# Performance work log

Measured on AMD Instinct MI355X. Metric: run time of the kernel, lower is better.

Reference implementation:

```python
import jax, jax.numpy as jnp
import numpy as np

D = 512
DB = D // 4          # 128
R = 4                # window radius
KB = 9               # boundary kernel
DH = D // 2          # attn mlp hidden
VOCABS = {"quality": 64, "root": 13, "bass": 13, "key": 25}
COMPS = ["quality", "root", "bass", "key"]
B, T = 4, 4096


def _ln(x, g, b, eps=1e-5):
    mu = jnp.mean(x, axis=-1, keepdims=True)
    var = jnp.var(x, axis=-1, keepdims=True)
    return (x - mu) * jax.lax.rsqrt(var + eps) * g + b


def setup_inputs() -> dict:
    key = jax.random.key(0)
    ks = jax.random.split(key, 24)
    s = 0.02
    inp = {
        "h": jax.random.normal(ks[0], (B, T, D), jnp.float32),
        # boundary head
        "w_bnd": jax.random.normal(ks[1], (D,), jnp.float32) * s,
        "b_bnd": jnp.zeros((1,), jnp.float32),
        # boundary smoother conv1d(1,1,KB)
        "conv_k": jax.random.normal(ks[2], (KB,), jnp.float32) * s,
        "conv_b": jnp.zeros((1,), jnp.float32),
        # FiLM boundary embeddings
        "e0": jnp.zeros((DB,), jnp.float32),
        "e1": jax.random.normal(ks[3], (DB,), jnp.float32) * s,
        # LayerNorms
        "ln_in_g": jnp.ones((D + DB,), jnp.float32),
        "ln_in_b": jnp.zeros((D + DB,), jnp.float32),
        "ln_h_g": jnp.ones((D,), jnp.float32),
        "ln_h_b": jnp.zeros((D,), jnp.float32),
        # FiLM mlp
        "film_w": jax.random.normal(ks[4], (D + DB, 2 * D), jnp.float32) * s,
        "film_b": jnp.zeros((2 * D,), jnp.float32),
        # per-component attn MLP (stacked over 4 comps)
        "attn_w1": jax.random.normal(ks[5], (4, D, DH), jnp.float32) * s,
        "attn_b1": jnp.zeros((4, DH), jnp.float32),
        "attn_w2": jax.random.normal(ks[6], (4, DH), jnp.float32) * s,
        "attn_b2": jnp.zeros((4,), jnp.float32),
        # per-component projector first layer (stacked)
        "proj_w1": jax.random.normal(ks[7], (4, D, D), jnp.float32) * s,
        "proj_b1": jnp.zeros((4, D), jnp.float32),
    }
    for i, c in enumerate(COMPS):
        inp[f"proj_w2_{c[0]}" if c != "key" else "proj_w2_k"] = jax.random.normal(ks[8 + i], (D, VOCABS[c]), jnp.float32) * s
        inp[f"proj_b2_{c[0]}" if c != "key" else "proj_b2_k"] = jnp.zeros((VOCABS[c],), jnp.float32)
    return inp


def reference(h, w_bnd, b_bnd, conv_k, conv_b, e0, e1,
              ln_in_g, ln_in_b, ln_h_g, ln_h_b, film_w, film_b,
              attn_w1, attn_b1, attn_w2, attn_b2, proj_w1, proj_b1,
              proj_w2_q, proj_b2_q, proj_w2_r, proj_b2_r,
              proj_w2_b, proj_b2_b, proj_w2_k, proj_b2_k):
    Bz, Tz, Dz = h.shape
    # boundary head + smoothing (conv1d, same padding) + sigmoid
    bl = jnp.einsum("btd,d->bt", h, w_bnd) + b_bnd[0]            # [B,T]
    sm = jax.lax.conv_general_dilated(bl[:, None, :], conv_k[None, None, :],
                                      (1,), [(KB // 2, KB // 2)]) + conv_b[0]
    b_soft = jax.nn.sigmoid(sm[:, 0, :])                          # [B,T]
    # FiLM
    eb = b_soft[..., None] * e1 + (1.0 - b_soft[..., None]) * e0  # [B,T,DB]
    film_in = _ln(jnp.concatenate([h, eb], axis=-1), ln_in_g, ln_in_b)
    gb = film_in @ film_w + film_b                                # [B,T,2D]
    gamma, beta = gb[..., :Dz], gb[..., Dz:]
    z = _ln(h, ln_h_g, ln_h_b) * (1.0 + gamma) + beta             # [B,T,D]
    # local windows via replicate pad + gather
    hp = jnp.pad(h, ((0, 0), (R, R), (0, 0)), mode="edge")        # [B,T+2R,D]
    idx = jnp.arange(Tz)[:, None] + jnp.arange(2 * R + 1)[None, :]  # [T,W]
    local = hp[:, idx, :]                                         # [B,T,W,D]
    c = jnp.concatenate([z[:, :, None, :], local], axis=2)        # [B,T,C,D]
    # attention pooling for all 4 components at once
    s1 = jax.nn.gelu(jnp.einsum("btcd,kdh->kbtch", c, attn_w1)
                     + attn_b1[:, None, None, None, :], approximate=False)
    scores = jnp.einsum("kbtch,kh->kbtc", s1, attn_w2) + attn_b2[:, None, None, None]
    attn = jax.nn.softmax(scores, axis=-1)                        # [K,B,T,C]
    pooled = jnp.einsum("kbtc,btcd->kbtd", attn, c)               # [K,B,T,D]
    p1 = jax.nn.gelu(jnp.einsum("kbtd,kde->kbte", pooled, proj_w1)
                     + proj_b1[:, None, None, :], approximate=False)
    lq = p1[0] @ proj_w2_q + proj_b2_q
    lr = p1[1] @ proj_w2_r + proj_b2_r
    lb = p1[2] @ proj_w2_b + proj_b2_b
    lk = p1[3] @ proj_w2_k + proj_b2_k
    return jnp.concatenate([lq, lr, lb, lk, bl[..., None]], axis=-1)  # [B,T,116]
```

## Files before the change

kernel.cpp:

```cpp
#include <hip/hip_runtime.h>
#include <hip/hip_bf16.h>

typedef unsigned short u16;
typedef unsigned int u32;

#define NR 16384
#define TT 4096

typedef __bf16 bf16_t;
typedef bf16_t bf16x8 __attribute__((ext_vector_type(8)));
typedef float f32x4 __attribute__((ext_vector_type(4)));

__device__ __forceinline__ float b2f(u16 u){ return __uint_as_float(((u32)u)<<16); }
__device__ __forceinline__ u16 f2b(float f){
  u32 u = __float_as_uint(f);
  u32 r = u + 0x7fffu + ((u>>16)&1u);
  return (u16)(r>>16);
}
__device__ __forceinline__ void up2(u32 u, float&a, float&b){
  a = __uint_as_float(u<<16);
  b = __uint_as_float(u & 0xffff0000u);
}
__device__ __forceinline__ void ld8(const u16* p, float* f){
  uint4 v = *(const uint4*)p;
  up2(v.x,f[0],f[1]); up2(v.y,f[2],f[3]);
  up2(v.z,f[4],f[5]); up2(v.w,f[6],f[7]);
}
__device__ __forceinline__ float wred(float v){
  #pragma unroll
  for(int o=32;o>0;o>>=1) v += __shfl_down(v,o,64);
  return v;
}
__device__ __forceinline__ float gelu_f(float x){
  float x2 = x*x;
  float u = x*(0.7978845608f + 0.0356774081f*x2);
  float e = __expf(2.0f*u);
  float t = 1.0f - 2.0f*__builtin_amdgcn_rcpf(e+1.0f);
  return 0.5f*x*(1.0f+t);
}
__device__ __forceinline__ void gl_lds(const void* g, void* l){
  __builtin_amdgcn_global_load_lds(
      (__attribute__((address_space(1))) void*)(void*)g,
      (__attribute__((address_space(3))) void*)l, 16, 0, 0);
}

__global__ void k_tw(const float* __restrict__ src, u16* __restrict__ dst,
                     int K, int N, long long sS, long long sD){
  __shared__ float t[32][33];
  const float* S = src + (size_t)blockIdx.z*sS;
  u16* D = dst + (size_t)blockIdx.z*sD;
  int k0 = blockIdx.y*32, n0 = blockIdx.x*32;
  int r = threadIdx.x>>5, c = threadIdx.x&31;
  #pragma unroll
  for(int p=0;p<4;p++) t[r+p*8][c] = S[(size_t)(k0+r+p*8)*N + n0 + c];
  __syncthreads();
  #pragma unroll
  for(int p=0;p<4;p++) D[(size_t)(n0+r+p*8)*K + k0 + c] = f2b(t[c][r+p*8]);
}

__global__ void k_w2c(const float* __restrict__ wq, const float* __restrict__ bq,
                      const float* __restrict__ wr, const float* __restrict__ br,
                      const float* __restrict__ wb_, const float* __restrict__ bb_,
                      const float* __restrict__ wk, const float* __restrict__ bk,
                      u16* __restrict__ W2c, float* __restrict__ b2c){
  int idx = blockIdx.x;
  int p = idx>>5, j = idx&31, tid = threadIdx.x;
  const float* Wm; const float* Bm; int V; int cofs = 0;
  if(p<=1){ Wm=wq; Bm=bq; V=64; cofs = p*32; }
  else if(p==2){ Wm=wr; Bm=br; V=13; }
  else if(p==3){ Wm=wb_; Bm=bb_; V=13; }
  else { Wm=wk; Bm=bk; V=25; }
  int c = j + cofs;
  bool valid = c < V;
  for(int k=tid;k<512;k+=256)
    W2c[(size_t)idx*512 + k] = f2b(valid ? Wm[(size_t)k*V + c] : 0.f);
  if(tid==0) b2c[idx] = valid ? Bm[c] : 0.f;
}

__global__ void k_esum(const float* __restrict__ e0, const float* __restrict__ e1,
                       float* __restrict__ es){
  int lane = threadIdx.x & 63;
  float x0 = e0[lane], x1 = e0[lane+64];
  float y0 = e1[lane], y1 = e1[lane+64];
  float s0 = x0+x1, s1 = y0+y1;
  float q0 = x0*x0+x1*x1, q1 = y0*y0+y1*y1, c = x0*y0+x1*y1;
  s0 = wred(s0); s1 = wred(s1); q0 = wred(q0); q1 = wred(q1); c = wred(c);
  if(lane==0){ es[0]=s0; es[1]=s1; es[2]=q0; es[3]=q1; es[4]=c; }
}

__global__ void k_bnd(const float* __restrict__ h, const float* __restrict__ wb,
                      const float* __restrict__ bb,
                      float* __restrict__ bl, float* __restrict__ hsum, float* __restrict__ hss,
                      u16* __restrict__ hbf, float* __restrict__ out){
  int wave = threadIdx.x>>6, lane = threadIdx.x&63;
  int n = blockIdx.x*4 + wave;
  const float4* hp = (const float4*)(h + (size_t)n*512 + lane*8);
  const float4* wp = (const float4*)(wb + lane*8);
  float4 h0 = hp[0], h1 = hp[1], w0 = wp[0], w1 = wp[1];
  float hv[8] = {h0.x,h0.y,h0.z,h0.w,h1.x,h1.y,h1.z,h1.w};
  float wv[8] = {w0.x,w0.y,w0.z,w0.w,w1.x,w1.y,w1.z,w1.w};
  float dot=0.f, s=0.f, ss=0.f;
  #pragma unroll
  for(int i=0;i<8;i++){ dot += hv[i]*wv[i]; s += hv[i]; ss += hv[i]*hv[i]; }
  u16* hd = hbf + (size_t)n*512 + lane*8;
  *(ushort4*)hd     = make_ushort4(f2b(hv[0]),f2b(hv[1]),f2b(hv[2]),f2b(hv[3]));
  *(ushort4*)(hd+4) = make_ushort4(f2b(hv[4]),f2b(hv[5]),f2b(hv[6]),f2b(hv[7]));
  dot = wred(dot); s = wred(s); ss = wred(ss);
  if(lane==0){
    float v = dot + bb[0];
    bl[n] = v; hsum[n]=s; hss[n]=ss;
    out[(size_t)n*116 + 115] = v;
  }
}

__global__ void k_conv(const float* __restrict__ bl, const float* __restrict__ ck,
                       const float* __restrict__ cb, float* __restrict__ bsoft){
  int n = blockIdx.x*256 + threadIdx.x;
  int b = n>>12, t = n&4095;
  float acc = cb[0];
  #pragma unroll
  for(int i=0;i<9;i++){
    int tt = t-4+i;
    if(tt>=0 && tt<TT) acc += bl[(b<<12)+tt]*ck[i];
  }
  bsoft[n] = 1.0f/(1.0f+expf(-acc));
}

__global__ void k_filmin(const u16* __restrict__ hbf, const float* __restrict__ bsoft,
                         const float* __restrict__ e0, const float* __restrict__ e1,
                         const float* __restrict__ es,
                         const float* __restrict__ hsum, const float* __restrict__ hss,
                         const float* __restrict__ g, const float* __restrict__ bb,
                         u16* __restrict__ fin){
  int n = blockIdx.x, tid = threadIdx.x;
  if(tid >= 160) return;
  float bs = bsoft[n], os = 1.0f - bs;
  float S  = hsum[n] + bs*es[1] + os*es[0];
  float SS = hss[n] + bs*bs*es[3] + 2.0f*bs*os*es[4] + os*os*es[2];
  float mu = S*(1.0f/640.0f);
  float var = SS*(1.0f/640.0f) - mu*mu;
  float rs = rsqrtf(var + 1e-5f);
  int d = tid*4;
  float v[4];
  if(d < 512){
    ushort4 hv = *(const ushort4*)(hbf + (size_t)n*512 + d);
    v[0]=b2f(hv.x); v[1]=b2f(hv.y); v[2]=b2f(hv.z); v[3]=b2f(hv.w);
  } else {
    float4 a = *(const float4*)(e1 + d - 512);
    float4 b0 = *(const float4*)(e0 + d - 512);
    v[0]=bs*a.x+os*b0.x; v[1]=bs*a.y+os*b0.y; v[2]=bs*a.z+os*b0.z; v[3]=bs*a.w+os*b0.w;
  }
  float4 g4 = *(const float4*)(g + d);
  float4 b4 = *(const float4*)(bb + d);
  u16 o[4];
  o[0]=f2b((v[0]-mu)*rs*g4.x+b4.x); o[1]=f2b((v[1]-mu)*rs*g4.y+b4.y);
  o[2]=f2b((v[2]-mu)*rs*g4.z+b4.z); o[3]=f2b((v[3]-mu)*rs*g4.w+b4.w);
  *(ushort4*)(fin + (size_t)n*640 + d) = make_ushort4(o[0],o[1],o[2],o[3]);
}

__global__ __launch_bounds__(256) void k_film(
    const u16* __restrict__ fin, const u16* __restrict__ WT, const float* __restrict__ fbias,
    const float* __restrict__ hsum, const float* __restrict__ hss,
    const float* __restrict__ lng, const float* __restrict__ lnb,
    const u16* __restrict__ hbf, u16* __restrict__ z){
  __shared__ __align__(16) u16 As[2][128*32];
  __shared__ __align__(16) u16 Bg[2][128*32];
  __shared__ __align__(16) u16 Bb2[2][128*32];
  int tid = threadIdx.x, wave = tid>>6, lane = tid&63;
  int cg0 = blockIdx.x*128, row0 = blockIdx.y*128;
  int wr = (wave>>1)*64, wc = (wave&1)*64;
  int lrow = lane>>2, lcol = (lane&3)*8, m15 = lane&15, q = lane>>4;
  f32x4 ag[4][4] = {}, ab[4][4] = {};
  for(int k0=0;k0<640;k0+=64){
    #pragma unroll
    for(int hh=0;hh<2;hh++){
      int kk = k0 + hh*32;
      const u16* ga = fin + (size_t)(row0 + wave*32 + lrow)*640 + kk + lcol;
      u16* la = &As[hh][wave*32*32];
      gl_lds(ga, la); gl_lds(ga + (size_t)16*640, la + 16*32);
      const u16* gg = WT + (size_t)(cg0 + wave*32 + lrow)*640 + kk + lcol;
      u16* lg = &Bg[hh][wave*32*32];
      gl_lds(gg, lg); gl_lds(gg + (size_t)16*640, lg + 16*32);
      const u16* gb2 = WT + (size_t)(cg0 + 512 + wave*32 + lrow)*640 + kk + lcol;
      u16* lb2 = &Bb2[hh][wave*32*32];
      gl_lds(gb2, lb2); gl_lds(gb2 + (size_t)16*640, lb2 + 16*32);
    }
    __syncthreads();
    #pragma unroll
    for(int hh=0;hh<2;hh++){
      bf16x8 af[4], bg[4], bb[4];
      #pragma unroll
      for(int i=0;i<4;i++){
        af[i] = *(const bf16x8*)&As[hh][(wr + i*16 + m15)*32 + q*8];
        bg[i] = *(const bf16x8*)&Bg[hh][(wc + i*16 + m15)*32 + q*8];
        bb[i] = *(const bf16x8*)&Bb2[hh][(wc + i*16 + m15)*32 + q*8];
      }
      #pragma unroll
      for(int i=0;i<4;i++)
        #pragma unroll
        for(int j=0;j<4;j++){
          ag[i][j] = __builtin_amdgcn_mfma_f32_16x16x32_bf16(bg[j], af[i], ag[i][j], 0,0,0);
          ab[i][j] = __builtin_amdgcn_mfma_f32_16x16x32_bf16(bb[j], af[i], ab[i][j], 0,0,0);
        }
    }
    __syncthreads();
  }
  #pragma unroll
  for(int i=0;i<4;i++){
    int m = row0 + wr + i*16 + m15;
    float mu = hsum[m]*(1.0f/512.0f);
    float var = hss[m]*(1.0f/512.0f) - mu*mu;
    float rs = rsqrtf(var + 1e-5f);
    #pragma unroll
    for(int j=0;j<4;j++){
      int d0 = cg0 + wc + j*16 + q*4;
      float4 g4 = *(const float4*)&lng[d0];
      float4 b4 = *(const float4*)&lnb[d0];
      float4 fg = *(const float4*)&fbias[d0];
      float4 fb = *(const float4*)&fbias[512+d0];
      float hv[4];
      { ushort4 hb4 = *(const ushort4*)(hbf + (size_t)m*512 + d0);
        hv[0]=b2f(hb4.x); hv[1]=b2f(hb4.y); hv[2]=b2f(hb4.z); hv[3]=b2f(hb4.w); }
      float gm[4] = {ag[i][j][0]+fg.x, ag[i][j][1]+fg.y, ag[i][j][2]+fg.z, ag[i][j][3]+fg.w};
      float bt[4] = {ab[i][j][0]+fb.x, ab[i][j][1]+fb.y, ab[i][j][2]+fb.z, ab[i][j][3]+fb.w};
      float gg4[4] = {g4.x,g4.y,g4.z,g4.w}, bb4[4] = {b4.x,b4.y,b4.z,b4.w};
      u16 o[4];
      #pragma unroll
      for(int r=0;r<4;r++){
        float ln = (hv[r]-mu)*rs*gg4[r] + bb4[r];
        o[r] = f2b(ln*(1.0f+gm[r]) + bt[r]);
      }
      *(ushort4*)(z + (size_t)m*512 + d0) = make_ushort4(o[0],o[1],o[2],o[3]);
    }
  }
}

__global__ __launch_bounds__(256) void k_msc(
    const u16* __restrict__ hb, const u16* __restrict__ zb,
    const u16* __restrict__ WT, const float* __restrict__ b1,
    const float* __restrict__ w2, float* __restrict__ sch, float* __restrict__ scz){
  __shared__ __align__(16) u16 As[2][64*32];
  __shared__ __align__(16) u16 Bs[2][256*32];
  int tid = threadIdx.x, wave = tid>>6, lane = tid&63;
  int bz = blockIdx.y, hk = bz>>1, src = bz&1;
  const u16* X = src ? zb : hb;
  float* sc = src ? scz : sch;
  int row0 = blockIdx.x*64;
  const u16* Wb = WT + (size_t)hk*256*512;
  int lrow = lane>>2, lcol = (lane&3)*8, m15 = lane&15, q = lane>>4;
  int wc = wave*64;
  f32x4 acc[4][4] = {};
  for(int k0=0;k0<512;k0+=64){
    #pragma unroll
    for(int hh=0;hh<2;hh++){
      int kk = k0 + hh*32;
      gl_lds(X + (size_t)(row0 + wave*16 + lrow)*512 + kk + lcol, &As[hh][wave*16*32]);
      #pragma unroll
      for(int r=0;r<4;r++)
        gl_lds(Wb + (size_t)(wave*64 + r*16 + lrow)*512 + kk + lcol,
               &Bs[hh][(wave*64 + r*16)*32]);
    }
    __syncthreads();
    #pragma unroll
    for(int hh=0;hh<2;hh++){
      bf16x8 af[4], bfr[4];
      #pragma unroll
      for(int i=0;i<4;i++){
        af[i]  = *(const bf16x8*)&As[hh][(i*16 + m15)*32 + q*8];
        bfr[i] = *(const bf16x8*)&Bs[hh][(wc + i*16 + m15)*32 + q*8];
      }
      #pragma unroll
      for(int i=0;i<4;i++)
        #pragma unroll
        for(int j=0;j<4;j++)
          acc[i][j] = __builtin_amdgcn_mfma_f32_16x16x32_bf16(bfr[j], af[i], acc[i][j], 0,0,0);
    }
    __syncthreads();
  }
  #pragma unroll
  for(int i=0;i<4;i++){
    float part = 0.f;
    #pragma unroll
    for(int j=0;j<4;j++){
      int n0 = wc + j*16 + q*4;
      float4 bias = *(const float4*)&b1[hk*256 + n0];
      float4 wv   = *(const float4*)&w2[hk*256 + n0];
      part += gelu_f(acc[i][j][0]+bias.x)*wv.x;
      part += gelu_f(acc[i][j][1]+bias.y)*wv.y;
      part += gelu_f(acc[i][j][2]+bias.z)*wv.z;
      part += gelu_f(acc[i][j][3]+bias.w)*wv.w;
    }
    part += __shfl_xor(part, 16, 64);
    part += __shfl_xor(part, 32, 64);
    if(q==0) atomicAdd(&sc[(size_t)hk*NR + row0 + i*16 + m15], part);
  }
}

__global__ __launch_bounds__(256) void k_proj(
    const u16* __restrict__ P, const u16* __restrict__ WT, const float* __restrict__ Bv,
    u16* __restrict__ X2){
  __shared__ __align__(16) u16 As[2][64*32];
  __shared__ __align__(16) u16 Bs[2][256*32];
  int tid = threadIdx.x, wave = tid>>6, lane = tid&63;
  int hk = blockIdx.z;
  int row0 = blockIdx.y*64, col0 = blockIdx.x*256;
  const u16* Xb = P + (size_t)hk*NR*512;
  const u16* Wb = WT + (size_t)hk*512*512 + (size_t)col0*512;
  const float* Bq = Bv + hk*512;
  int lrow = lane>>2, lcol = (lane&3)*8, m15 = lane&15, q = lane>>4;
  int wc = wave*64;
  f32x4 acc[4][4] = {};
  for(int k0=0;k0<512;k0+=64){
    #pragma unroll
    for(int hh=0;hh<2;hh++){
      int kk = k0 + hh*32;
      gl_lds(Xb + (size_t)(row0 + wave*16 + lrow)*512 + kk + lcol, &As[hh][wave*16*32]);
      #pragma unroll
      for(int r=0;r<4;r++)
        gl_lds(Wb + (size_t)(wave*64 + r*16 + lrow)*512 + kk + lcol,
               &Bs[hh][(wave*64 + r*16)*32]);
    }
    __syncthreads();
    #pragma unroll
    for(int hh=0;hh<2;hh++){
      bf16x8 af[4], bfr[4];
      #pragma unroll
      for(int i=0;i<4;i++){
        af[i]  = *(const bf16x8*)&As[hh][(i*16 + m15)*32 + q*8];
        bfr[i] = *(const bf16x8*)&Bs[hh][(wc + i*16 + m15)*32 + q*8];
      }
      #pragma unroll
      for(int i=0;i<4;i++)
        #pragma unroll
        for(int j=0;j<4;j++)
          acc[i][j] = __builtin_amdgcn_mfma_f32_16x16x32_bf16(bfr[j], af[i], acc[i][j], 0,0,0);
    }
    __syncthreads();
  }
  #pragma unroll
  for(int i=0;i<4;i++){
    size_t mrow = (size_t)(row0 + i*16 + m15)*2048 + hk*512;
    #pragma unroll
    for(int j=0;j<4;j++){
      int n0 = col0 + wc + j*16 + q*4;
      float4 bias = *(const float4*)&Bq[n0];
      float v0 = gelu_f(acc[i][j][0] + bias.x);
      float v1 = gelu_f(acc[i][j][1] + bias.y);
      float v2 = gelu_f(acc[i][j][2] + bias.z);
      float v3 = gelu_f(acc[i][j][3] + bias.w);
      *(ushort4*)(X2 + mrow + n0) = make_ushort4(f2b(v0),f2b(v1),f2b(v2),f2b(v3));
    }
  }
}

__global__ __launch_bounds__(256) void k_f2(
    const u16* __restrict__ X2, const u16* __restrict__ W2c, const float* __restrict__ b2c,
    float* __restrict__ out){
  __shared__ __align__(16) u16 As[2][128*32];
  __shared__ __align__(16) u16 Bs[2][32*32];
  int tid = threadIdx.x, wave = tid>>6, lane = tid&63;
  int row0 = blockIdx.x*128, p = blockIdx.y;
  int hk = (p<=1)?0:(p-1);
  int B0 = (p==0)?0:(p==1)?32:(p==2)?64:(p==3)?77:90;
  int V  = (p<=1)?32:(p==4)?25:13;
  int lrow = lane>>2, lcol = (lane&3)*8, m15 = lane&15, q = lane>>4;
  f32x4 acc[2][2] = {};
  for(int k0=0;k0<512;k0+=64){
    #pragma unroll
    for(int hh=0;hh<2;hh++){
      int kk = k0 + hh*32;
      const u16* ga = X2 + (size_t)(row0 + wave*32 + lrow)*2048 + hk*512 + kk + lcol;
      u16* la = &As[hh][wave*32*32];
      gl_lds(ga, la);
      gl_lds(ga + (size_t)16*2048, la + 16*32);
      if(wave<2)
        gl_lds(W2c + (size_t)(p*32 + wave*16 + lrow)*512 + kk + lcol, &Bs[hh][wave*16*32]);
    }
    __syncthreads();
    #pragma unroll
    for(int hh=0;hh<2;hh++){
      bf16x8 af[2], bfr[2];
      #pragma unroll
      for(int i=0;i<2;i++) af[i] = *(const bf16x8*)&As[hh][(wave*32 + i*16 + m15)*32 + q*8];
      #pragma unroll
      for(int j=0;j<2;j++) bfr[j] = *(const bf16x8*)&Bs[hh][(j*16+m15)*32 + q*8];
      #pragma unroll
      for(int i=0;i<2;i++)
        #pragma unroll
        for(int j=0;j<2;j++)
          acc[i][j] = __builtin_amdgcn_mfma_f32_16x16x32_bf16(bfr[j], af[i], acc[i][j], 0,0,0);
    }
    __syncthreads();
  }
  #pragma unroll
  for(int i=0;i<2;i++){
    size_t mrow = (size_t)(row0 + wave*32 + i*16 + m15)*116;
    #pragma unroll
    for(int j=0;j<2;j++){
      int nl0 = j*16 + q*4;
      #pragma unroll
      for(int r=0;r<4;r++){
        int nl = nl0 + r;
        if(nl < V) out[mrow + B0 + nl] = acc[i][j][r] + b2c[p*32+nl];
      }
    }
  }
}

__global__ __launch_bounds__(256) void k_pool(
    const u16* __restrict__ hb, const u16* __restrict__ z,
    const float* __restrict__ sch, const float* __restrict__ scz,
    u16* __restrict__ P){
  int wave = threadIdx.x>>6, lane = threadIdx.x&63;
  int n = blockIdx.x*4 + wave;
  int b = n>>12, t = n&4095;
  int k = lane&3, j = lane>>2;
  float s;
  if(j==0) s = scz[(size_t)k*NR+n];
  else if(j<10){
    int tc = t-5+j; tc = tc<0?0:(tc>TT-1?TT-1:tc);
    s = sch[(size_t)k*NR + (b<<12) + tc];
  } else s = -1e30f;
  float m = s;
  #pragma unroll
  for(int o=4;o<64;o<<=1) m = fmaxf(m, __shfl_xor(m,o,64));
  float e = (j<10)? expf(s-m) : 0.f;
  float sum = e;
  #pragma unroll
  for(int o=4;o<64;o<<=1) sum += __shfl_xor(sum,o,64);
  float ev = e/sum;
  int d0 = lane*8;
  float acc[4][8] = {};
  #pragma unroll
  for(int jj=0;jj<10;jj++){
    const u16* src;
    if(jj==0) src = z + (size_t)n*512 + d0;
    else {
      int tc = t-5+jj; tc = tc<0?0:(tc>TT-1?TT-1:tc);
      src = hb + ((size_t)(b<<12)+tc)*512 + d0;
    }
    float f[8]; ld8(src, f);
    float w0 = __shfl(ev, jj*4+0, 64);
    float w1 = __shfl(ev, jj*4+1, 64);
    float w2 = __shfl(ev, jj*4+2, 64);
    float w3 = __shfl(ev, jj*4+3, 64);
    #pragma unroll
    for(int i=0;i<8;i++){
      acc[0][i] += w0*f[i];
      acc[1][i] += w1*f[i];
      acc[2][i] += w2*f[i];
      acc[3][i] += w3*f[i];
    }
  }
  #pragma unroll
  for(int kk=0;kk<4;kk++){
    u16* dst = P + ((size_t)kk*NR + n)*512 + d0;
    *(ushort4*)dst     = make_ushort4(f2b(acc[kk][0]),f2b(acc[kk][1]),f2b(acc[kk][2]),f2b(acc[kk][3]));
    *(ushort4*)(dst+4) = make_ushort4(f2b(acc[kk][4]),f2b(acc[kk][5]),f2b(acc[kk][6]),f2b(acc[kk][7]));
  }
}

#define OFF_BL     0u
#define OFF_BSOFT  65536u
#define OFF_HSUM   131072u
#define OFF_HSS    196608u
#define OFF_SCH    262144u
#define OFF_SCZ    524288u
#define OFF_FIN    786432u
#define OFF_Z      55312384u
#define OFF_HBF    72089600u
#define OFF_WF     88866816u
#define OFF_WA     90177536u
#define OFF_WP     91226112u
#define OFF_P      93323264u
#define OFF_W2C    160432128u
#define OFF_B2C    160595968u
#define OFF_ES     160596608u

extern "C" void kernel_launch(void* const* d_in, const int* in_sizes, int n_in,
                              void* d_out, int out_size, void* d_ws, size_t ws_size,
                              hipStream_t stream){
  const float* h       = (const float*)d_in[0];
  const float* w_bnd   = (const float*)d_in[1];
  const float* b_bnd   = (const float*)d_in[2];
  const float* conv_k  = (const float*)d_in[3];
  const float* conv_b  = (const float*)d_in[4];
  const float* e0      = (const float*)d_in[5];
  const float* e1      = (const float*)d_in[6];
  const float* ln_in_g = (const float*)d_in[7];
  const float* ln_in_b = (const float*)d_in[8];
  const float* ln_h_g  = (const float*)d_in[9];
  const float* ln_h_b  = (const float*)d_in[10];
  const float* film_w  = (const float*)d_in[11];
  const float* film_b  = (const float*)d_in[12];
  const float* attn_w1 = (const float*)d_in[13];
  const float* attn_b1 = (const float*)d_in[14];
  const float* attn_w2 = (const float*)d_in[15];
  const float* proj_w1 = (const float*)d_in[17];
  const float* proj_b1 = (const float*)d_in[18];
  const float* wq = (const float*)d_in[19];
  const float* bq = (const float*)d_in[20];
  const float* wr = (const float*)d_in[21];
  const float* br = (const float*)d_in[22];
  const float* wb_ = (const float*)d_in[23];
  const float* bb_ = (const float*)d_in[24];
  const float* wk = (const float*)d_in[25];
  const float* bk = (const float*)d_in[26];
  float* out = (float*)d_out;
  char* ws = (char*)d_ws;

  float* bl    = (float*)(ws + OFF_BL);
  float* bsoft = (float*)(ws + OFF_BSOFT);
  float* hsum  = (float*)(ws + OFF_HSUM);
  float* hss   = (float*)(ws + OFF_HSS);
  float* sch   = (float*)(ws + OFF_SCH);
  float* scz   = (float*)(ws + OFF_SCZ);
  u16* fin     = (u16*)(ws + OFF_FIN);
  u16* X2      = (u16*)(ws + OFF_FIN);
  u16* z       = (u16*)(ws + OFF_Z);
  u16* hbf     = (u16*)(ws + OFF_HBF);
  u16* wfilm   = (u16*)(ws + OFF_WF);
  u16* wattn   = (u16*)(ws + OFF_WA);
  u16* wproj   = (u16*)(ws + OFF_WP);
  u16* P       = (u16*)(ws + OFF_P);
  u16* w2c     = (u16*)(ws + OFF_W2C);
  float* b2c   = (float*)(ws + OFF_B2C);
  float* es    = (float*)(ws + OFF_ES);

  hipMemsetAsync(ws + OFF_SCH, 0, 524288, stream);

  {
    dim3 g(1024/32, 640/32, 1);
    k_tw<<<g,256,0,stream>>>(film_w, wfilm, 640, 1024, 0, 0);
  }
  {
    dim3 g(256/32, 512/32, 4);
    k_tw<<<g,256,0,stream>>>(attn_w1, wattn, 512, 256, 512LL*256, 256LL*512);
  }
  {
    dim3 g(512/32, 512/32, 4);
    k_tw<<<g,256,0,stream>>>(proj_w1, wproj, 512, 512, 512LL*512, 512LL*512);
  }
  k_w2c<<<160,256,0,stream>>>(wq,bq,wr,br,wb_,bb_,wk,bk, w2c, b2c);
  k_esum<<<1,64,0,stream>>>(e0, e1, es);

  k_bnd<<<NR/4,256,0,stream>>>(h,w_bnd,b_bnd,bl,hsum,hss,hbf,out);
  k_conv<<<NR/256,256,0,stream>>>(bl,conv_k,conv_b,bsoft);
  k_filmin<<<NR,256,0,stream>>>(hbf,bsoft,e0,e1,es,hsum,hss,ln_in_g,ln_in_b,fin);

  {
    dim3 g(4, NR/128);
    k_film<<<g,256,0,stream>>>(fin, wfilm, film_b, hsum, hss, ln_h_g, ln_h_b, hbf, z);
  }

  {
    dim3 g(NR/64, 8);
    k_msc<<<g,256,0,stream>>>(hbf, z, wattn, attn_b1, attn_w2, sch, scz);
  }

  k_pool<<<NR/4,256,0,stream>>>(hbf,z,sch,scz,P);

  {
    dim3 g(2, NR/64, 4);
    k_proj<<<g,256,0,stream>>>(P, wproj, proj_b1, X2);
  }

  {
    dim3 g(NR/128, 5);
    k_f2<<<g,256,0,stream>>>(X2, w2c, b2c, out);
  }
}
```

Measured before the change: 387.5 us.

## Fuse projector second layer into k_proj and drop score atomics/memset

The projector's second GEMM is now computed inside k_proj. Each block covers all 512 hidden columns in two halves, stages the GELU output in LDS, and multiplies it by the small per-component output weights. This removes the X2 global round-trip and the separate k_f2 launch. k_msc now reduces its per-wave partial scores in LDS and writes them directly instead of using atomicAdd, so the memset of the score buffer goes away. In exchange k_proj has half as many blocks, more LDS, a serialized second-layer stage with W2c read straight from global, and redundant A-tile loads across the two halves.

```diff
diff --git a/kernel.cpp b/kernel.cpp
--- a/kernel.cpp
+++ b/kernel.cpp
@@ -241,6 +241,7 @@
     const float* __restrict__ w2, float* __restrict__ sch, float* __restrict__ scz){
   __shared__ __align__(16) u16 As[2][64*32];
   __shared__ __align__(16) u16 Bs[2][256*32];
+  __shared__ float pw[4][64];
   int tid = threadIdx.x, wave = tid>>6, lane = tid&63;
   int bz = blockIdx.y, hk = bz>>1, src = bz&1;
   const u16* X = src ? zb : hb;
@@ -292,116 +293,102 @@
     }
     part += __shfl_xor(part, 16, 64);
     part += __shfl_xor(part, 32, 64);
-    if(q==0) atomicAdd(&sc[(size_t)hk*NR + row0 + i*16 + m15], part);
+    if(q==0) pw[wave][i*16 + m15] = part;
+  }
+  __syncthreads();
+  if(tid < 64){
+    float s = pw[0][tid] + pw[1][tid] + pw[2][tid] + pw[3][tid];
+    sc[(size_t)hk*NR + row0 + tid] = s;
   }
 }
 
 __global__ __launch_bounds__(256) void k_proj(
     const u16* __restrict__ P, const u16* __restrict__ WT, const float* __restrict__ Bv,
-    u16* __restrict__ X2){
+    const u16* __restrict__ W2c, const float* __restrict__ b2c,
+    float* __restrict__ out){
   __shared__ __align__(16) u16 As[2][64*32];
-  __shared__ __align__(16) u16 Bs[2][256*32];
+  __shared__ __align__(16) u16 BsS[16896];
   int tid = threadIdx.x, wave = tid>>6, lane = tid&63;
-  int hk = blockIdx.z;
-  int row0 = blockIdx.y*64, col0 = blockIdx.x*256;
+  int hk = blockIdx.y;
+  int row0 = blockIdx.x*64;
   const u16* Xb = P + (size_t)hk*NR*512;
-  const u16* Wb = WT + (size_t)hk*512*512 + (size_t)col0*512;
   const float* Bq = Bv + hk*512;
+  int r2base = (hk==0) ? 0 : (hk+1)*32;
+  int nt = (hk==0) ? 4 : 2;
+  int B0 = (hk==0)?0:(hk==1)?64:(hk==2)?77:90;
+  int V  = (hk==0)?64:(hk==3)?25:13;
   int lrow = lane>>2, lcol = (lane&3)*8, m15 = lane&15, q = lane>>4;
   int wc = wave*64;
-  f32x4 acc[4][4] = {};
-  for(int k0=0;k0<512;k0+=64){
-    #pragma unroll
-    for(int hh=0;hh<2;hh++){
-      int kk = k0 + hh*32;
-      gl_lds(Xb + (size_t)(row0 + wave*16 + lrow)*512 + kk + lcol, &As[hh][wave*16*32]);
-      #pragma unroll
-      for(int r=0;r<4;r++)
-        gl_lds(Wb + (size_t)(wave*64 + r*16 + lrow)*512 + kk + lcol,
-               &Bs[hh][(wave*64 + r*16)*32]);
+  f32x4 acc2[4] = {};
+  for(int half=0; half<2; half++){
+    int c0 = half*256;
+    const u16* Wb = WT + (size_t)hk*512*512 + (size_t)c0*512;
+    f32x4 acc[4][4] = {};
+    for(int k0=0;k0<512;k0+=64){
+      #pragma unroll
+      for(int hh=0;hh<2;hh++){
+        int kk = k0 + hh*32;
+        gl_lds(Xb + (size_t)(row0 + wave*16 + lrow)*512 + kk + lcol, &As[hh][wave*16*32]);
+        u16* lb = &BsS[hh*256*32 + wave*64*32];
+        #pragma unroll
+        for(int r=0;r<4;r++)
+          gl_lds(Wb + (size_t)(wave*64 + r*16 + lrow)*512 + kk + lcol, lb + r*16*32);
+      }
+      __syncthreads();
+      #pragma unroll
+      for(int hh=0;hh<2;hh++){
+        bf16x8 af[4], bfr[4];
+        #pragma unroll
+        for(int i=0;i<4;i++){
+          af[i]  = *(const bf16x8*)&As[hh][(i*16 + m15)*32 + q*8];
+          bfr[i] = *(const bf16x8*)&BsS[hh*256*32 + (wc + i*16 + m15)*32 + q*8];
+        }
+        #pragma unroll
+        for(int i=0;i<4;i++)
+          #pragma unroll
+          for(int j=0;j<4;j++)
+            acc[i][j] = __builtin_amdgcn_mfma_f32_16x16x32_bf16(bfr[j], af[i], acc[i][j], 0,0,0);
+      }
+      __syncthreads();
+    }
+    #pragma unroll
+    for(int i=0;i<4;i++){
+      int srow = i*16 + m15;
+      #pragma unroll
+      for(int j=0;j<4;j++){
+        int sn = wc + j*16 + q*4;
+        float4 bias = *(const float4*)&Bq[c0 + sn];
+        float v0 = gelu_f(acc[i][j][0] + bias.x);
+        float v1 = gelu_f(acc[i][j][1] + bias.y);
+        float v2 = gelu_f(acc[i][j][2] + bias.z);
+        float v3 = gelu_f(acc[i][j][3] + bias.w);
+        *(ushort4*)&BsS[srow*264 + sn] = make_ushort4(f2b(v0),f2b(v1),f2b(v2),f2b(v3));
+      }
     }
     __syncthreads();
-    #pragma unroll
-    for(int hh=0;hh<2;hh++){
-      bf16x8 af[4], bfr[4];
-      #pragma unroll
-      for(int i=0;i<4;i++){
-        af[i]  = *(const bf16x8*)&As[hh][(i*16 + m15)*32 + q*8];
-        bfr[i] = *(const bf16x8*)&Bs[hh][(wc + i*16 + m15)*32 + q*8];
-      }
-      #pragma unroll
-      for(int i=0;i<4;i++)
+    for(int k2=0;k2<256;k2+=32){
+      bf16x8 af2 = *(const bf16x8*)&BsS[(wave*16 + m15)*264 + k2 + q*8];
+      #pragma unroll
+      for(int j=0;j<4;j++){
+        if(j<nt){
+          bf16x8 bf2 = *(const bf16x8*)&W2c[(size_t)(r2base + j*16 + m15)*512 + c0 + k2 + q*8];
+          acc2[j] = __builtin_amdgcn_mfma_f32_16x16x32_bf16(af2, bf2, acc2[j], 0,0,0);
+        }
+      }
+    }
+    __syncthreads();
+  }
+  #pragma unroll
+  for(int j=0;j<4;j++){
+    if(j<nt){
+      int n = j*16 + m15;
+      if(n < V){
+        float bias = b2c[r2base + n];
         #pragma unroll
-        for(int j=0;j<4;j++)
-          acc[i][j] = __builtin_amdgcn_mfma_f32_16x16x32_bf16(bfr[j], af[i], acc[i][j], 0,0,0);
-    }
-    __syncthreads();
-  }
-  #pragma unroll
-  for(int i=0;i<4;i++){
-    size_t mrow = (size_t)(row0 + i*16 + m15)*2048 + hk*512;
-    #pragma unroll
-    for(int j=0;j<4;j++){
-      int n0 = col0 + wc + j*16 + q*4;
-      float4 bias = *(const float4*)&Bq[n0];
-      float v0 = gelu_f(acc[i][j][0] + bias.x);
-      float v1 = gelu_f(acc[i][j][1] + bias.y);
-      float v2 = gelu_f(acc[i][j][2] + bias.z);
-      float v3 = gelu_f(acc[i][j][3] + bias.w);
-      *(ushort4*)(X2 + mrow + n0) = make_ushort4(f2b(v0),f2b(v1),f2b(v2),f2b(v3));
-    }
-  }
-}
-
-__global__ __launch_bounds__(256) void k_f2(
-    const u16* __restrict__ X2, const u16* __restrict__ W2c, const float* __restrict__ b2c,
-    float* __restrict__ out){
-  __shared__ __align__(16) u16 As[2][128*32];
-  __shared__ __align__(16) u16 Bs[2][32*32];
-  int tid = threadIdx.x, wave = tid>>6, lane = tid&63;
-  int row0 = blockIdx.x*128, p = blockIdx.y;
-  int hk = (p<=1)?0:(p-1);
-  int B0 = (p==0)?0:(p==1)?32:(p==2)?64:(p==3)?77:90;
-  int V  = (p<=1)?32:(p==4)?25:13;
-  int lrow = lane>>2, lcol = (lane&3)*8, m15 = lane&15, q = lane>>4;
-  f32x4 acc[2][2] = {};
-  for(int k0=0;k0<512;k0+=64){
-    #pragma unroll
-    for(int hh=0;hh<2;hh++){
-      int kk = k0 + hh*32;
-      const u16* ga = X2 + (size_t)(row0 + wave*32 + lrow)*2048 + hk*512 + kk + lcol;
-      u16* la = &As[hh][wave*32*32];
-      gl_lds(ga, la);
-      gl_lds(ga + (size_t)16*2048, la + 16*32);
-      if(wave<2)
-        gl_lds(W2c + (size_t)(p*32 + wave*16 + lrow)*512 + kk + lcol, &Bs[hh][wave*16*32]);
-    }
-    __syncthreads();
-    #pragma unroll
-    for(int hh=0;hh<2;hh++){
-      bf16x8 af[2], bfr[2];
-      #pragma unroll
-      for(int i=0;i<2;i++) af[i] = *(const bf16x8*)&As[hh][(wave*32 + i*16 + m15)*32 + q*8];
-      #pragma unroll
-      for(int j=0;j<2;j++) bfr[j] = *(const bf16x8*)&Bs[hh][(j*16+m15)*32 + q*8];
-      #pragma unroll
-      for(int i=0;i<2;i++)
-        #pragma unroll
-        for(int j=0;j<2;j++)
-          acc[i][j] = __builtin_amdgcn_mfma_f32_16x16x32_bf16(bfr[j], af[i], acc[i][j], 0,0,0);
-    }
-    __syncthreads();
-  }
-  #pragma unroll
-  for(int i=0;i<2;i++){
-    size_t mrow = (size_t)(row0 + wave*32 + i*16 + m15)*116;
-    #pragma unroll
-    for(int j=0;j<2;j++){
-      int nl0 = j*16 + q*4;
-      #pragma unroll
-      for(int r=0;r<4;r++){
-        int nl = nl0 + r;
-        if(nl < V) out[mrow + B0 + nl] = acc[i][j][r] + b2c[p*32+nl];
+        for(int r=0;r<4;r++){
+          int row = row0 + wave*16 + q*4 + r;
+          out[(size_t)row*116 + B0 + n] = acc2[j][r] + bias;
+        }
       }
     }
   }
@@ -516,7 +503,6 @@
   float* sch   = (float*)(ws + OFF_SCH);
   float* scz   = (float*)(ws + OFF_SCZ);
   u16* fin     = (u16*)(ws + OFF_FIN);
-  u16* X2      = (u16*)(ws + OFF_FIN);
   u16* z       = (u16*)(ws + OFF_Z);
   u16* hbf     = (u16*)(ws + OFF_HBF);
   u16* wfilm   = (u16*)(ws + OFF_WF);
@@ -527,8 +513,6 @@
   float* b2c   = (float*)(ws + OFF_B2C);
   float* es    = (float*)(ws + OFF_ES);
 
-  hipMemsetAsync(ws + OFF_SCH, 0, 524288, stream);
-
   {
     dim3 g(1024/32, 640/32, 1);
     k_tw<<<g,256,0,stream>>>(film_w, wfilm, 640, 1024, 0, 0);
@@ -561,12 +545,7 @@
   k_pool<<<NR/4,256,0,stream>>>(hbf,z,sch,scz,P);
 
   {
-    dim3 g(2, NR/64, 4);
-    k_proj<<<g,256,0,stream>>>(P, wproj, proj_b1, X2);
-  }
-
-  {
-    dim3 g(NR/128, 5);
-    k_f2<<<g,256,0,stream>>>(X2, w2c, b2c, out);
-  }
-}
+    dim3 g(NR/64, 4);
+    k_proj<<<g,256,0,stream>>>(P, wproj, proj_b1, w2c, b2c, out);
+  }
+}
```

New measurement: 442.8 us. 1.14x slower.

## Software-pipeline GEMM main loops with register prefetch and drop score atomics

Applied to the files above, without the earlier changes.

The k_msc and k_proj GEMM loops previously loaded directly global-to-LDS and synchronized before computing. They now prefetch the next K-slice into registers while running MFMAs on the current LDS buffer, then store the prefetched slice to the alternate LDS buffer. That overlaps global latency with compute, at the cost of more registers and a narrower per-iteration K step. The score reduction now combines the four waves' partials in shared memory and writes them directly instead of using atomicAdd. This removes the workspace memset and the atomic traffic.

```diff
diff --git a/kernel.cpp b/kernel.cpp
--- a/kernel.cpp
+++ b/kernel.cpp
@@ -241,6 +241,7 @@
     const float* __restrict__ w2, float* __restrict__ sch, float* __restrict__ scz){
   __shared__ __align__(16) u16 As[2][64*32];
   __shared__ __align__(16) u16 Bs[2][256*32];
+  __shared__ float pw[4][64];
   int tid = threadIdx.x, wave = tid>>6, lane = tid&63;
   int bz = blockIdx.y, hk = bz>>1, src = bz&1;
   const u16* X = src ? zb : hb;
@@ -249,31 +250,50 @@
   const u16* Wb = WT + (size_t)hk*256*512;
   int lrow = lane>>2, lcol = (lane&3)*8, m15 = lane&15, q = lane>>4;
   int wc = wave*64;
+  const u16* gA = X + (size_t)(row0 + wave*16 + lrow)*512 + lcol;
+  const u16* gB = Wb + (size_t)(wave*64 + lrow)*512 + lcol;
+  int aoff = (wave*16 + lrow)*32 + lcol;
+  int boff = (wave*64 + lrow)*32 + lcol;
+  uint4 ra  = *(const uint4*)gA;
+  uint4 rb0 = *(const uint4*)(gB);
+  uint4 rb1 = *(const uint4*)(gB + 16*512);
+  uint4 rb2 = *(const uint4*)(gB + 32*512);
+  uint4 rb3 = *(const uint4*)(gB + 48*512);
+  *(uint4*)&As[0][aoff] = ra;
+  *(uint4*)&Bs[0][boff]        = rb0;
+  *(uint4*)&Bs[0][boff+16*32]  = rb1;
+  *(uint4*)&Bs[0][boff+32*32]  = rb2;
+  *(uint4*)&Bs[0][boff+48*32]  = rb3;
+  __syncthreads();
   f32x4 acc[4][4] = {};
-  for(int k0=0;k0<512;k0+=64){
-    #pragma unroll
-    for(int hh=0;hh<2;hh++){
-      int kk = k0 + hh*32;
-      gl_lds(X + (size_t)(row0 + wave*16 + lrow)*512 + kk + lcol, &As[hh][wave*16*32]);
-      #pragma unroll
-      for(int r=0;r<4;r++)
-        gl_lds(Wb + (size_t)(wave*64 + r*16 + lrow)*512 + kk + lcol,
-               &Bs[hh][(wave*64 + r*16)*32]);
-    }
-    __syncthreads();
-    #pragma unroll
-    for(int hh=0;hh<2;hh++){
-      bf16x8 af[4], bfr[4];
-      #pragma unroll
-      for(int i=0;i<4;i++){
-        af[i]  = *(const bf16x8*)&As[hh][(i*16 + m15)*32 + q*8];
-        bfr[i] = *(const bf16x8*)&Bs[hh][(wc + i*16 + m15)*32 + q*8];
-      }
-      #pragma unroll
-      for(int i=0;i<4;i++)
-        #pragma unroll
-        for(int j=0;j<4;j++)
-          acc[i][j] = __builtin_amdgcn_mfma_f32_16x16x32_bf16(bfr[j], af[i], acc[i][j], 0,0,0);
+  for(int it=0; it<16; it++){
+    int cur = it&1;
+    if(it<15){
+      int k0 = (it+1)*32;
+      ra  = *(const uint4*)(gA + k0);
+      rb0 = *(const uint4*)(gB + k0);
+      rb1 = *(const uint4*)(gB + 16*512 + k0);
+      rb2 = *(const uint4*)(gB + 32*512 + k0);
+      rb3 = *(const uint4*)(gB + 48*512 + k0);
+    }
+    bf16x8 af[4], bfr[4];
+    #pragma unroll
+    for(int i=0;i<4;i++){
+      af[i]  = *(const bf16x8*)&As[cur][(i*16 + m15)*32 + q*8];
+      bfr[i] = *(const bf16x8*)&Bs[cur][(wc + i*16 + m15)*32 + q*8];
+    }
+    #pragma unroll
+    for(int i=0;i<4;i++)
+      #pragma unroll
+      for(int j=0;j<4;j++)
+        acc[i][j] = __builtin_amdgcn_mfma_f32_16x16x32_bf16(bfr[j], af[i], acc[i][j], 0,0,0);
+    if(it<15){
+      int nxt = cur^1;
+      *(uint4*)&As[nxt][aoff] = ra;
+      *(uint4*)&Bs[nxt][boff]        = rb0;
+      *(uint4*)&Bs[nxt][boff+16*32]  = rb1;
+      *(uint4*)&Bs[nxt][boff+32*32]  = rb2;
+      *(uint4*)&Bs[nxt][boff+48*32]  = rb3;
     }
     __syncthreads();
   }
@@ -292,7 +312,12 @@
     }
     part += __shfl_xor(part, 16, 64);
     part += __shfl_xor(part, 32, 64);
-    if(q==0) atomicAdd(&sc[(size_t)hk*NR + row0 + i*16 + m15], part);
+    if(q==0) pw[wave][i*16 + m15] = part;
+  }
+  __syncthreads();
+  if(tid < 64){
+    float s = pw[0][tid] + pw[1][tid] + pw[2][tid] + pw[3][tid];
+    sc[(size_t)hk*NR + row0 + tid] = s;
   }
 }
 
@@ -309,31 +334,50 @@
   const float* Bq = Bv + hk*512;
   int lrow = lane>>2, lcol = (lane&3)*8, m15 = lane&15, q = lane>>4;
   int wc = wave*64;
+  const u16* gA = Xb + (size_t)(row0 + wave*16 + lrow)*512 + lcol;
+  const u16* gB = Wb + (size_t)(wave*64 + lrow)*512 + lcol;
+  int aoff = (wave*16 + lrow)*32 + lcol;
+  int boff = (wave*64 + lrow)*32 + lcol;
+  uint4 ra  = *(const uint4*)gA;
+  uint4 rb0 = *(const uint4*)(gB);
+  uint4 rb1 = *(const uint4*)(gB + 16*512);
+  uint4 rb2 = *(const uint4*)(gB + 32*512);
+  uint4 rb3 = *(const uint4*)(gB + 48*512);
+  *(uint4*)&As[0][aoff] = ra;
+  *(uint4*)&Bs[0][boff]        = rb0;
+  *(uint4*)&Bs[0][boff+16*32]  = rb1;
+  *(uint4*)&Bs[0][boff+32*32]  = rb2;
+  *(uint4*)&Bs[0][boff+48*32]  = rb3;
+  __syncthreads();
   f32x4 acc[4][4] = {};
-  for(int k0=0;k0<512;k0+=64){
-    #pragma unroll
-    for(int hh=0;hh<2;hh++){
-      int kk = k0 + hh*32;
-      gl_lds(Xb + (size_t)(row0 + wave*16 + lrow)*512 + kk + lcol, &As[hh][wave*16*32]);
-      #pragma unroll
-      for(int r=0;r<4;r++)
-        gl_lds(Wb + (size_t)(wave*64 + r*16 + lrow)*512 + kk + lcol,
-               &Bs[hh][(wave*64 + r*16)*32]);
-    }
-    __syncthreads();
-    #pragma unroll
-    for(int hh=0;hh<2;hh++){
-      bf16x8 af[4], bfr[4];
-      #pragma unroll
-      for(int i=0;i<4;i++){
-        af[i]  = *(const bf16x8*)&As[hh][(i*16 + m15)*32 + q*8];
-        bfr[i] = *(const bf16x8*)&Bs[hh][(wc + i*16 + m15)*32 + q*8];
-      }
-      #pragma unroll
-      for(int i=0;i<4;i++)
-        #pragma unroll
-        for(int j=0;j<4;j++)
-          acc[i][j] = __builtin_amdgcn_mfma_f32_16x16x32_bf16(bfr[j], af[i], acc[i][j], 0,0,0);
+  for(int it=0; it<16; it++){
+    int cur = it&1;
+    if(it<15){
+      int k0 = (it+1)*32;
+      ra  = *(const uint4*)(gA + k0);
+      rb0 = *(const uint4*)(gB + k0);
+      rb1 = *(const uint4*)(gB + 16*512 + k0);
+      rb2 = *(const uint4*)(gB + 32*512 + k0);
+      rb3 = *(const uint4*)(gB + 48*512 + k0);
+    }
+    bf16x8 af[4], bfr[4];
+    #pragma unroll
+    for(int i=0;i<4;i++){
+      af[i]  = *(const bf16x8*)&As[cur][(i*16 + m15)*32 + q*8];
+      bfr[i] = *(const bf16x8*)&Bs[cur][(wc + i*16 + m15)*32 + q*8];
+    }
+    #pragma unroll
+    for(int i=0;i<4;i++)
+      #pragma unroll
+      for(int j=0;j<4;j++)
+        acc[i][j] = __builtin_amdgcn_mfma_f32_16x16x32_bf16(bfr[j], af[i], acc[i][j], 0,0,0);
+    if(it<15){
+      int nxt = cur^1;
+      *(uint4*)&As[nxt][aoff] = ra;
+      *(uint4*)&Bs[nxt][boff]        = rb0;
+      *(uint4*)&Bs[nxt][boff+16*32]  = rb1;
+      *(uint4*)&Bs[nxt][boff+32*32]  = rb2;
+      *(uint4*)&Bs[nxt][boff+48*32]  = rb3;
     }
     __syncthreads();
   }
@@ -527,8 +571,6 @@
   float* b2c   = (float*)(ws + OFF_B2C);
   float* es    = (float*)(ws + OFF_ES);
 
-  hipMemsetAsync(ws + OFF_SCH, 0, 524288, stream);
-
   {
     dim3 g(1024/32, 640/32, 1);
     k_tw<<<g,256,0,stream>>>(film_w, wfilm, 640, 1024, 0, 0);
```

Result: no change. 381.7 us (-1.5%).

## Load MFMA operands straight from global into registers, drop LDS staging and atomics

Applied to the files above, without the earlier changes.

Three GEMM kernels (attention score, projector, final logits) now load their MFMA fragments directly from global memory into registers with a two-stage software prefetch. This removes the LDS staging buffers and the block-wide barriers on every K step. The score kernel also reduces per-wave partial sums in shared memory and writes each row once, so the zeroing memset and the global atomics go away. The cost is that every wave now fetches its own copy of the shared A tile from global/L2, and the B tile is read without reuse across waves. The per-lane 16-byte row-strided loads are also less coalesced than the previous LDS fills.

```diff
diff --git a/kernel.cpp b/kernel.cpp
--- a/kernel.cpp
+++ b/kernel.cpp
@@ -239,43 +239,51 @@
     const u16* __restrict__ hb, const u16* __restrict__ zb,
     const u16* __restrict__ WT, const float* __restrict__ b1,
     const float* __restrict__ w2, float* __restrict__ sch, float* __restrict__ scz){
-  __shared__ __align__(16) u16 As[2][64*32];
-  __shared__ __align__(16) u16 Bs[2][256*32];
+  __shared__ float pw[4][64];
   int tid = threadIdx.x, wave = tid>>6, lane = tid&63;
   int bz = blockIdx.y, hk = bz>>1, src = bz&1;
   const u16* X = src ? zb : hb;
   float* sc = src ? scz : sch;
   int row0 = blockIdx.x*64;
   const u16* Wb = WT + (size_t)hk*256*512;
-  int lrow = lane>>2, lcol = (lane&3)*8, m15 = lane&15, q = lane>>4;
+  int m15 = lane&15, q = lane>>4;
   int wc = wave*64;
+  const u16* pA = X  + (size_t)(row0 + m15)*512 + q*8;
+  const u16* pB = Wb + (size_t)(wc   + m15)*512 + q*8;
+  uint4 rA0[4], rB0[4], rA1[4], rB1[4];
+  #pragma unroll
+  for(int i=0;i<4;i++){
+    rA0[i] = *(const uint4*)(pA + (size_t)i*16*512);
+    rB0[i] = *(const uint4*)(pB + (size_t)i*16*512);
+  }
   f32x4 acc[4][4] = {};
-  for(int k0=0;k0<512;k0+=64){
-    #pragma unroll
-    for(int hh=0;hh<2;hh++){
-      int kk = k0 + hh*32;
-      gl_lds(X + (size_t)(row0 + wave*16 + lrow)*512 + kk + lcol, &As[hh][wave*16*32]);
-      #pragma unroll
-      for(int r=0;r<4;r++)
-        gl_lds(Wb + (size_t)(wave*64 + r*16 + lrow)*512 + kk + lcol,
-               &Bs[hh][(wave*64 + r*16)*32]);
-    }
-    __syncthreads();
-    #pragma unroll
-    for(int hh=0;hh<2;hh++){
-      bf16x8 af[4], bfr[4];
+  for(int it=0; it<16; it+=2){
+    int k1 = (it+1)*32;
+    #pragma unroll
+    for(int i=0;i<4;i++){
+      rA1[i] = *(const uint4*)(pA + (size_t)i*16*512 + k1);
+      rB1[i] = *(const uint4*)(pB + (size_t)i*16*512 + k1);
+    }
+    #pragma unroll
+    for(int i=0;i<4;i++)
+      #pragma unroll
+      for(int j=0;j<4;j++)
+        acc[i][j] = __builtin_amdgcn_mfma_f32_16x16x32_bf16(
+            *(const bf16x8*)&rB0[j], *(const bf16x8*)&rA0[i], acc[i][j], 0,0,0);
+    if(it+2<16){
+      int k2 = (it+2)*32;
       #pragma unroll
       for(int i=0;i<4;i++){
-        af[i]  = *(const bf16x8*)&As[hh][(i*16 + m15)*32 + q*8];
-        bfr[i] = *(const bf16x8*)&Bs[hh][(wc + i*16 + m15)*32 + q*8];
+        rA0[i] = *(const uint4*)(pA + (size_t)i*16*512 + k2);
+        rB0[i] = *(const uint4*)(pB + (size_t)i*16*512 + k2);
       }
-      #pragma unroll
-      for(int i=0;i<4;i++)
-        #pragma unroll
-        for(int j=0;j<4;j++)
-          acc[i][j] = __builtin_amdgcn_mfma_f32_16x16x32_bf16(bfr[j], af[i], acc[i][j], 0,0,0);
-    }
-    __syncthreads();
+    }
+    #pragma unroll
+    for(int i=0;i<4;i++)
+      #pragma unroll
+      for(int j=0;j<4;j++)
+        acc[i][j] = __builtin_amdgcn_mfma_f32_16x16x32_bf16(
+            *(const bf16x8*)&rB1[j], *(const bf16x8*)&rA1[i], acc[i][j], 0,0,0);
   }
   #pragma unroll
   for(int i=0;i<4;i++){
@@ -292,50 +300,62 @@
     }
     part += __shfl_xor(part, 16, 64);
     part += __shfl_xor(part, 32, 64);
-    if(q==0) atomicAdd(&sc[(size_t)hk*NR + row0 + i*16 + m15], part);
+    if(q==0) pw[wave][i*16 + m15] = part;
+  }
+  __syncthreads();
+  if(tid < 64){
+    float s = pw[0][tid] + pw[1][tid] + pw[2][tid] + pw[3][tid];
+    sc[(size_t)hk*NR + row0 + tid] = s;
   }
 }
 
 __global__ __launch_bounds__(256) void k_proj(
     const u16* __restrict__ P, const u16* __restrict__ WT, const float* __restrict__ Bv,
     u16* __restrict__ X2){
-  __shared__ __align__(16) u16 As[2][64*32];
-  __shared__ __align__(16) u16 Bs[2][256*32];
   int tid = threadIdx.x, wave = tid>>6, lane = tid&63;
   int hk = blockIdx.z;
   int row0 = blockIdx.y*64, col0 = blockIdx.x*256;
   const u16* Xb = P + (size_t)hk*NR*512;
   const u16* Wb = WT + (size_t)hk*512*512 + (size_t)col0*512;
   const float* Bq = Bv + hk*512;
-  int lrow = lane>>2, lcol = (lane&3)*8, m15 = lane&15, q = lane>>4;
+  int m15 = lane&15, q = lane>>4;
   int wc = wave*64;
+  const u16* pA = Xb + (size_t)(row0 + m15)*512 + q*8;
+  const u16* pB = Wb + (size_t)(wc   + m15)*512 + q*8;
+  uint4 rA0[4], rB0[4], rA1[4], rB1[4];
+  #pragma unroll
+  for(int i=0;i<4;i++){
+    rA0[i] = *(const uint4*)(pA + (size_t)i*16*512);
+    rB0[i] = *(const uint4*)(pB + (size_t)i*16*512);
+  }
   f32x4 acc[4][4] = {};
-  for(int k0=0;k0<512;k0+=64){
-    #pragma unroll
-    for(int hh=0;hh<2;hh++){
-      int kk = k0 + hh*32;
-      gl_lds(Xb + (size_t)(row0 + wave*16 + lrow)*512 + kk + lcol, &As[hh][wave*16*32]);
-      #pragma unroll
-      for(int r=0;r<4;r++)
-        gl_lds(Wb + (size_t)(wave*64 + r*16 + lrow)*512 + kk + lcol,
-               &Bs[hh][(wave*64 + r*16)*32]);
-    }
-    __syncthreads();
-    #pragma unroll
-    for(int hh=0;hh<2;hh++){
-      bf16x8 af[4], bfr[4];
+  for(int it=0; it<16; it+=2){
+    int k1 = (it+1)*32;
+    #pragma unroll
+    for(int i=0;i<4;i++){
+      rA1[i] = *(const uint4*)(pA + (size_t)i*16*512 + k1);
+      rB1[i] = *(const uint4*)(pB + (size_t)i*16*512 + k1);
+    }
+    #pragma unroll
+    for(int i=0;i<4;i++)
+      #pragma unroll
+      for(int j=0;j<4;j++)
+        acc[i][j] = __builtin_amdgcn_mfma_f32_16x16x32_bf16(
+            *(const bf16x8*)&rB0[j], *(const bf16x8*)&rA0[i], acc[i][j], 0,0,0);
+    if(it+2<16){
+      int k2 = (it+2)*32;
       #pragma unroll
       for(int i=0;i<4;i++){
-        af[i]  = *(const bf16x8*)&As[hh][(i*16 + m15)*32 + q*8];
-        bfr[i] = *(const bf16x8*)&Bs[hh][(wc + i*16 + m15)*32 + q*8];
+        rA0[i] = *(const uint4*)(pA + (size_t)i*16*512 + k2);
+        rB0[i] = *(const uint4*)(pB + (size_t)i*16*512 + k2);
       }
-      #pragma unroll
-      for(int i=0;i<4;i++)
-        #pragma unroll
-        for(int j=0;j<4;j++)
-          acc[i][j] = __builtin_amdgcn_mfma_f32_16x16x32_bf16(bfr[j], af[i], acc[i][j], 0,0,0);
-    }
-    __syncthreads();
+    }
+    #pragma unroll
+    for(int i=0;i<4;i++)
+      #pragma unroll
+      for(int j=0;j<4;j++)
+        acc[i][j] = __builtin_amdgcn_mfma_f32_16x16x32_bf16(
+            *(const bf16x8*)&rB1[j], *(const bf16x8*)&rA1[i], acc[i][j], 0,0,0);
   }
   #pragma unroll
   for(int i=0;i<4;i++){
@@ -356,41 +376,48 @@
 __global__ __launch_bounds__(256) void k_f2(
     const u16* __restrict__ X2, const u16* __restrict__ W2c, const float* __restrict__ b2c,
     float* __restrict__ out){
-  __shared__ __align__(16) u16 As[2][128*32];
-  __shared__ __align__(16) u16 Bs[2][32*32];
   int tid = threadIdx.x, wave = tid>>6, lane = tid&63;
   int row0 = blockIdx.x*128, p = blockIdx.y;
   int hk = (p<=1)?0:(p-1);
   int B0 = (p==0)?0:(p==1)?32:(p==2)?64:(p==3)?77:90;
   int V  = (p<=1)?32:(p==4)?25:13;
-  int lrow = lane>>2, lcol = (lane&3)*8, m15 = lane&15, q = lane>>4;
+  int m15 = lane&15, q = lane>>4;
+  const u16* pA = X2  + (size_t)(row0 + wave*32 + m15)*2048 + hk*512 + q*8;
+  const u16* pB = W2c + (size_t)(p*32 + m15)*512 + q*8;
+  uint4 rA0[2], rB0[2], rA1[2], rB1[2];
+  #pragma unroll
+  for(int i=0;i<2;i++){
+    rA0[i] = *(const uint4*)(pA + (size_t)i*16*2048);
+    rB0[i] = *(const uint4*)(pB + (size_t)i*16*512);
+  }
   f32x4 acc[2][2] = {};
-  for(int k0=0;k0<512;k0+=64){
-    #pragma unroll
-    for(int hh=0;hh<2;hh++){
-      int kk = k0 + hh*32;
-      const u16* ga = X2 + (size_t)(row0 + wave*32 + lrow)*2048 + hk*512 + kk + lcol;
-      u16* la = &As[hh][wave*32*32];
-      gl_lds(ga, la);
-      gl_lds(ga + (size_t)16*2048, la + 16*32);
-      if(wave<2)
-        gl_lds(W2c + (size_t)(p*32 + wave*16 + lrow)*512 + kk + lcol, &Bs[hh][wave*16*32]);
-    }
-    __syncthreads();
-    #pragma unroll
-    for(int hh=0;hh<2;hh++){
-      bf16x8 af[2], bfr[2];
-      #pragma unroll
-      for(int i=0;i<2;i++) af[i] = *(const bf16x8*)&As[hh][(wave*32 + i*16 + m15)*32 + q*8];
-      #pragma unroll
-      for(int j=0;j<2;j++) bfr[j] = *(const bf16x8*)&Bs[hh][(j*16+m15)*32 + q*8];
-      #pragma unroll
-      for(int i=0;i<2;i++)
-        #pragma unroll
-        for(int j=0;j<2;j++)
-          acc[i][j] = __builtin_amdgcn_mfma_f32_16x16x32_bf16(bfr[j], af[i], acc[i][j], 0,0,0);
-    }
-    __syncthreads();
+  for(int it=0; it<16; it+=2){
+    int k1 = (it+1)*32;
+    #pragma unroll
+    for(int i=0;i<2;i++){
+      rA1[i] = *(const uint4*)(pA + (size_t)i*16*2048 + k1);
+      rB1[i] = *(const uint4*)(pB + (size_t)i*16*512 + k1);
+    }
+    #pragma unroll
+    for(int i=0;i<2;i++)
+      #pragma unroll
+      for(int j=0;j<2;j++)
+        acc[i][j] = __builtin_amdgcn_mfma_f32_16x16x32_bf16(
+            *(const bf16x8*)&rB0[j], *(const bf16x8*)&rA0[i], acc[i][j], 0,0,0);
+    if(it+2<16){
+      int k2 = (it+2)*32;
+      #pragma unroll
+      for(int i=0;i<2;i++){
+        rA0[i] = *(const uint4*)(pA + (size_t)i*16*2048 + k2);
+        rB0[i] = *(const uint4*)(pB + (size_t)i*16*512 + k2);
+      }
+    }
+    #pragma unroll
+    for(int i=0;i<2;i++)
+      #pragma unroll
+      for(int j=0;j<2;j++)
+        acc[i][j] = __builtin_amdgcn_mfma_f32_16x16x32_bf16(
+            *(const bf16x8*)&rB1[j], *(const bf16x8*)&rA1[i], acc[i][j], 0,0,0);
   }
   #pragma unroll
   for(int i=0;i<2;i++){
@@ -527,8 +554,6 @@
   float* b2c   = (float*)(ws + OFF_B2C);
   float* es    = (float*)(ws + OFF_ES);
 
-  hipMemsetAsync(ws + OFF_SCH, 0, 524288, stream);
-
   {
     dim3 g(1024/32, 640/32, 1);
     k_tw<<<g,256,0,stream>>>(film_w, wfilm, 640, 1024, 0, 0);
```

Measured after the change: 518.8 us. 1.34x slower.
